# Performance work log

Measured on AMD Instinct MI355X. Metric: run time of the kernel, lower is better.

The kernel has to match this reference:

```python
import jax, jax.numpy as jnp
import numpy as np

B, S, H, I, E, K = 2, 2048, 1024, 2048, 8, 2


def setup_inputs() -> dict:
    key = jax.random.key(0)
    k1, k2, k3, k4, k5 = jax.random.split(key, 5)
    scale_h = 1.0 / np.sqrt(H)
    scale_i = 1.0 / np.sqrt(I)
    return {
        "x": jax.random.normal(k1, (B, S, H), dtype=jnp.float32),
        "Wg": jax.random.normal(k2, (H, E), dtype=jnp.float32) * scale_h,
        "W11": jax.random.normal(k3, (E, H, I), dtype=jnp.float32) * scale_h,
        "W12": jax.random.normal(k4, (E, H, I), dtype=jnp.float32) * scale_h,
        "W2": jax.random.normal(k5, (E, I, H), dtype=jnp.float32) * scale_i,
    }


def reference(x, Wg, W11, W12, W2):
    # Router: softmax over experts, then top-k with renormalization (+1e-8 as in torch ref)
    gate_scores = jax.nn.softmax(x @ Wg, axis=-1)          # [B,S,E]
    topk_scores, topk_idx = jax.lax.top_k(gate_scores, K)   # [B,S,K]
    topk_scores = topk_scores / (topk_scores.sum(-1, keepdims=True) + 1e-8)

    # Dense per-expert SwiGLU on all tokens (matches reference's masked-dense math)
    gate = jnp.einsum('bsh,ehi->bsei', x, W11)              # [B,S,E,I]
    value = jnp.einsum('bsh,ehi->bsei', x, W12)
    fused = (gate * jax.nn.sigmoid(gate)) * value           # SiLU(gate) * value
    expert_out = jnp.einsum('bsei,eih->bseh', fused, W2)    # [B,S,E,H]

    # Gather the top-k experts' outputs per token and combine with routing weights
    gathered = jnp.take_along_axis(expert_out, topk_idx[..., None], axis=2)  # [B,S,K,H]
    out = jnp.sum(topk_scores[..., None] * gathered, axis=2)                 # [B,S,H]
    return out
```

## Files before the change

### kernel.cpp

```cpp
#include <hip/hip_runtime.h>
#include <hip/hip_bf16.h>
#include <stdint.h>

#define B_ 2
#define S_ 2048
#define H_ 1024
#define I_ 2048
#define E_ 8
#define TOK (B_*S_)
#define PAIRS (TOK*2)
#define MAXBLK 80

typedef __bf16 bf16_t;
typedef __bf16 bf16x4 __attribute__((ext_vector_type(4)));
typedef __bf16 bf16x8 __attribute__((ext_vector_type(8)));
typedef float  f32x4  __attribute__((ext_vector_type(4)));
typedef float  f32x16 __attribute__((ext_vector_type(16)));

__device__ __forceinline__ void gl_lds16(const bf16_t* g, bf16_t* l) {
    __builtin_amdgcn_global_load_lds(
        (const __attribute__((address_space(1))) unsigned int*)g,
        (__attribute__((address_space(3))) unsigned int*)l, 16, 0, 0);
}

__global__ void router_kernel(const float* __restrict__ x, const float* __restrict__ Wg,
                              int* __restrict__ top2e, float* __restrict__ top2w,
                              int* __restrict__ counts) {
    int wave = threadIdx.x >> 6;
    int lane = threadIdx.x & 63;
    int t = blockIdx.x * 4 + wave;
    if (t >= TOK) return;
    float acc[E_];
#pragma unroll
    for (int e = 0; e < E_; e++) acc[e] = 0.f;
    const float* xrow = x + (size_t)t * H_;
    for (int j = 0; j < H_ / 64; j++) {
        int h = j * 64 + lane;
        float xv = xrow[h];
        const float4* wg = (const float4*)(Wg + (size_t)h * E_);
        float4 w0 = wg[0], w1 = wg[1];
        acc[0] += xv * w0.x; acc[1] += xv * w0.y; acc[2] += xv * w0.z; acc[3] += xv * w0.w;
        acc[4] += xv * w1.x; acc[5] += xv * w1.y; acc[6] += xv * w1.z; acc[7] += xv * w1.w;
    }
#pragma unroll
    for (int e = 0; e < E_; e++) {
#pragma unroll
        for (int m = 32; m >= 1; m >>= 1) acc[e] += __shfl_xor(acc[e], m, 64);
    }
    if (lane == 0) {
        float mx = acc[0];
        for (int e = 1; e < E_; e++) mx = fmaxf(mx, acc[e]);
        float p[E_]; float z = 0.f;
        for (int e = 0; e < E_; e++) { p[e] = __expf(acc[e] - mx); z += p[e]; }
        for (int e = 0; e < E_; e++) p[e] /= z;
        int i1 = 0; float p1 = p[0];
        for (int e = 1; e < E_; e++) if (p[e] > p1) { p1 = p[e]; i1 = e; }
        int i2 = -1; float p2 = -1.f;
        for (int e = 0; e < E_; e++) if (e != i1 && p[e] > p2) { p2 = p[e]; i2 = e; }
        float s = p1 + p2 + 1e-8f;
        top2e[t * 2]     = i1; top2e[t * 2 + 1] = i2;
        top2w[t * 2]     = p1 / s; top2w[t * 2 + 1] = p2 / s;
        atomicAdd(&counts[i1], 1);
        atomicAdd(&counts[i2], 1);
    }
}

__global__ void scan_kernel(const int* __restrict__ counts, int* __restrict__ offsets,
                            int* __restrict__ cursor, int* __restrict__ blk_e,
                            int* __restrict__ blk_m0, int* __restrict__ nblk) {
    if (threadIdx.x == 0 && blockIdx.x == 0) {
        int run = 0, b = 0;
        for (int e = 0; e < E_; e++) {
            offsets[e] = run; cursor[e] = run;
            int c = counts[e];
            for (int m0 = 0; m0 < c; m0 += 128) { blk_e[b] = e; blk_m0[b] = m0; b++; }
            run += c;
        }
        nblk[0] = b;
    }
}

__global__ void fill_kernel(const int* __restrict__ top2e,
                            int* __restrict__ cursor, int* __restrict__ pair_tok,
                            int* __restrict__ inv) {
    int t = blockIdx.x * blockDim.x + threadIdx.x;
    if (t >= TOK) return;
#pragma unroll
    for (int k = 0; k < 2; k++) {
        int e = top2e[t * 2 + k];
        int pos = atomicAdd(&cursor[e], 1);
        pair_tok[pos] = t;
        inv[t * 2 + k] = pos;
    }
}

__global__ void castx_kernel(const float* __restrict__ x, bf16_t* __restrict__ xb) {
    size_t i = ((size_t)blockIdx.x * blockDim.x + threadIdx.x) * 4;
    float4 v = *(const float4*)(x + i);
    bf16x4 o = { (bf16_t)v.x, (bf16_t)v.y, (bf16_t)v.z, (bf16_t)v.w };
    *(bf16x4*)(xb + i) = o;
}

__global__ __launch_bounds__(256) void transpose_cast_kernel(
    const float* __restrict__ src, bf16_t* __restrict__ dst, int R, int C) {
    __shared__ float tile[64][129];
    int e = blockIdx.z;
    const float* s = src + (size_t)e * R * C;
    bf16_t* d = dst + (size_t)e * R * C;
    int c0 = blockIdx.x * 128, r0 = blockIdx.y * 64;
    int t = threadIdx.x;
#pragma unroll
    for (int j = 0; j < 8; j++) {
        int flat = j * 256 + t;
        int r = flat >> 5;
        int c4 = (flat & 31) * 4;
        float4 v = *(const float4*)(s + (size_t)(r0 + r) * C + c0 + c4);
        tile[r][c4 + 0] = v.x;
        tile[r][c4 + 1] = v.y;
        tile[r][c4 + 2] = v.z;
        tile[r][c4 + 3] = v.w;
    }
    __syncthreads();
#pragma unroll
    for (int j = 0; j < 4; j++) {
        int flat = j * 256 + t;
        int orow = flat >> 3;
        int seg  = (flat & 7) * 8;
        bf16x8 v;
#pragma unroll
        for (int k = 0; k < 8; k++) v[k] = (bf16_t)tile[seg + k][orow];
        *(bf16x8*)(d + (size_t)(c0 + orow) * R + r0 + seg) = v;
    }
}

__global__ __launch_bounds__(256, 2) void gemm1_kernel(
    const bf16_t* __restrict__ xb,
    const bf16_t* __restrict__ W11t,
    const bf16_t* __restrict__ W12t,
    const int* __restrict__ counts, const int* __restrict__ offsets,
    const int* __restrict__ blk_e, const int* __restrict__ blk_m0,
    const int* __restrict__ nblk,
    const int* __restrict__ pair_tok,
    bf16_t* __restrict__ fused)
{
    int by = blockIdx.y;
    if (by >= nblk[0]) return;
    int e = blk_e[by];
    int m0 = blk_m0[by];
    int cnt = counts[e];
    int off = offsets[e];
    int n0 = blockIdx.x * 128;

    __shared__ __align__(16) bf16_t la[128 * 64];
    __shared__ __align__(16) bf16_t lb[256 * 64];

    int tid = threadIdx.x;
    int w = tid >> 6, lane = tid & 63;
    int wm = w >> 1, wn = w & 1;
    int lrow = lane >> 3, lcol = lane & 7;
    int scol = lcol ^ lrow;

    const bf16_t* aptr4[4];
    const bf16_t* bptr[8];
#pragma unroll
    for (int it = 0; it < 4; it++) {
        int r = it * 32 + w * 8 + lrow;
        int grow = m0 + r;
        int tok = pair_tok[off + (grow < cnt ? grow : 0)];
        aptr4[it] = xb + (size_t)tok * H_ + scol * 8;
    }
#pragma unroll
    for (int it = 0; it < 8; it++) {
        int r = it * 32 + w * 8 + lrow;
        const bf16_t* base = (r < 128)
            ? (W11t + ((size_t)e * I_ + n0 + r) * H_)
            : (W12t + ((size_t)e * I_ + n0 + (r - 128)) * H_);
        bptr[it] = base + scol * 8;
    }

    f32x16 acc[2][4];
#pragma unroll
    for (int a = 0; a < 2; a++)
#pragma unroll
        for (int b = 0; b < 4; b++) acc[a][b] = (f32x16)(0.f);

    int r32 = lane & 31;
    int khalf = lane >> 5;
    int rx = r32 & 7;

    for (int k0 = 0; k0 < H_; k0 += 64) {
#pragma unroll
        for (int it = 0; it < 4; it++)
            gl_lds16(aptr4[it] + k0, &la[(it * 32 + w * 8) * 64]);
#pragma unroll
        for (int it = 0; it < 8; it++)
            gl_lds16(bptr[it] + k0, &lb[(it * 32 + w * 8) * 64]);
        __syncthreads();
#pragma unroll
        for (int t16 = 0; t16 < 4; t16++) {
            int seg = t16 * 2 + khalf;
            bf16x8 af[2], bfr[4];
#pragma unroll
            for (int ms = 0; ms < 2; ms++) {
                int row = wm * 64 + ms * 32 + r32;
                af[ms] = *(const bf16x8*)&la[row * 64 + (seg ^ rx) * 8];
            }
#pragma unroll
            for (int ns = 0; ns < 2; ns++) {
                int browg = wn * 64 + ns * 32 + r32;
                bfr[ns]     = *(const bf16x8*)&lb[browg * 64 + (seg ^ rx) * 8];
                bfr[ns + 2] = *(const bf16x8*)&lb[(browg + 128) * 64 + (seg ^ rx) * 8];
            }
#pragma unroll
            for (int ms = 0; ms < 2; ms++)
#pragma unroll
                for (int ns = 0; ns < 4; ns++)
                    acc[ms][ns] = __builtin_amdgcn_mfma_f32_32x32x16_bf16(
                        af[ms], bfr[ns], acc[ms][ns], 0, 0, 0);
        }
        __syncthreads();
    }

#pragma unroll
    for (int ms = 0; ms < 2; ms++) {
#pragma unroll
        for (int ns = 0; ns < 2; ns++) {
            int i = n0 + wn * 64 + ns * 32 + r32;
#pragma unroll
            for (int reg = 0; reg < 16; reg++) {
                int rrow = (reg & 3) + 8 * (reg >> 2) + 4 * khalf;
                int grow = m0 + wm * 64 + ms * 32 + rrow;
                if (grow < cnt) {
                    float g = acc[ms][ns][reg];
                    float v = acc[ms][ns + 2][reg];
                    float f = g * v / (1.f + __expf(-g));
                    fused[(size_t)(off + grow) * I_ + i] = (bf16_t)f;
                }
            }
        }
    }
}

__global__ __launch_bounds__(256, 3) void gemm2_kernel(
    const bf16_t* __restrict__ fused,
    const bf16_t* __restrict__ W2t,
    const int* __restrict__ counts, const int* __restrict__ offsets,
    const int* __restrict__ blk_e, const int* __restrict__ blk_m0,
    const int* __restrict__ nblk,
    float* __restrict__ y)
{
    int by = blockIdx.y;
    if (by >= nblk[0]) return;
    int e = blk_e[by];
    int m0 = blk_m0[by];
    int cnt = counts[e];
    int off = offsets[e];
    int n0 = blockIdx.x * 128;

    __shared__ __align__(16) bf16_t la[128 * 64];
    __shared__ __align__(16) bf16_t lb[128 * 64];

    int tid = threadIdx.x;
    int w = tid >> 6, lane = tid & 63;
    int wm = w >> 1, wn = w & 1;
    int lrow = lane >> 3, lcol = lane & 7;
    int scol = lcol ^ lrow;

    const bf16_t* aptr[4];
    const bf16_t* bptr[4];
#pragma unroll
    for (int it = 0; it < 4; it++) {
        int r = it * 32 + w * 8 + lrow;
        int grow = m0 + r;
        if (grow >= cnt) grow = cnt - 1;
        aptr[it] = fused + (size_t)(off + grow) * I_ + scol * 8;
        bptr[it] = W2t + ((size_t)e * H_ + n0 + r) * I_ + scol * 8;
    }

    f32x16 acc[2][2];
#pragma unroll
    for (int a = 0; a < 2; a++)
#pragma unroll
        for (int b = 0; b < 2; b++) acc[a][b] = (f32x16)(0.f);

    int r32 = lane & 31;
    int khalf = lane >> 5;
    int rx = r32 & 7;

    for (int k0 = 0; k0 < I_; k0 += 64) {
#pragma unroll
        for (int it = 0; it < 4; it++) {
            gl_lds16(aptr[it] + k0, &la[(it * 32 + w * 8) * 64]);
            gl_lds16(bptr[it] + k0, &lb[(it * 32 + w * 8) * 64]);
        }
        __syncthreads();
#pragma unroll
        for (int t16 = 0; t16 < 4; t16++) {
            int seg = t16 * 2 + khalf;
            bf16x8 af[2], bfr[2];
#pragma unroll
            for (int ms = 0; ms < 2; ms++) {
                int row = wm * 64 + ms * 32 + r32;
                af[ms] = *(const bf16x8*)&la[row * 64 + (seg ^ rx) * 8];
            }
#pragma unroll
            for (int ns = 0; ns < 2; ns++) {
                int brow = wn * 64 + ns * 32 + r32;
                bfr[ns] = *(const bf16x8*)&lb[brow * 64 + (seg ^ rx) * 8];
            }
#pragma unroll
            for (int ms = 0; ms < 2; ms++)
#pragma unroll
                for (int ns = 0; ns < 2; ns++)
                    acc[ms][ns] = __builtin_amdgcn_mfma_f32_32x32x16_bf16(
                        af[ms], bfr[ns], acc[ms][ns], 0, 0, 0);
        }
        __syncthreads();
    }

#pragma unroll
    for (int ms = 0; ms < 2; ms++) {
#pragma unroll
        for (int reg = 0; reg < 16; reg++) {
            int rrow = (reg & 3) + 8 * (reg >> 2) + 4 * khalf;
            int grow = m0 + wm * 64 + ms * 32 + rrow;
            if (grow < cnt) {
                int slot = off + grow;
#pragma unroll
                for (int ns = 0; ns < 2; ns++) {
                    int h = n0 + wn * 64 + ns * 32 + r32;
                    y[(size_t)slot * H_ + h] = acc[ms][ns][reg];
                }
            }
        }
    }
}

__global__ __launch_bounds__(256) void combine_kernel(
    const float* __restrict__ y, const int* __restrict__ inv,
    const float* __restrict__ top2w, float* __restrict__ out) {
    int t = blockIdx.x;
    int h = threadIdx.x * 4;
    int s1 = inv[t * 2], s2 = inv[t * 2 + 1];
    float w1 = top2w[t * 2], w2 = top2w[t * 2 + 1];
    f32x4 a = *(const f32x4*)(y + (size_t)s1 * H_ + h);
    f32x4 b = *(const f32x4*)(y + (size_t)s2 * H_ + h);
    f32x4 r = a * w1 + b * w2;
    *(f32x4*)(out + (size_t)t * H_ + h) = r;
}

extern "C" void kernel_launch(void* const* d_in, const int* in_sizes, int n_in,
                              void* d_out, int out_size, void* d_ws, size_t ws_size,
                              hipStream_t stream) {
    const float* x   = (const float*)d_in[0];
    const float* Wg  = (const float*)d_in[1];
    const float* W11 = (const float*)d_in[2];
    const float* W12 = (const float*)d_in[3];
    const float* W2  = (const float*)d_in[4];
    float* out = (float*)d_out;

    char* ws = (char*)d_ws;
    size_t o = 0;
    auto alloc = [&](size_t bytes) { size_t r = o; o = (o + bytes + 255) & ~(size_t)255; return r; };
    int*    counts   = (int*)(ws + alloc(E_ * 4));
    int*    offsets  = (int*)(ws + alloc(E_ * 4));
    int*    cursor   = (int*)(ws + alloc(E_ * 4));
    int*    blk_e    = (int*)(ws + alloc(MAXBLK * 4));
    int*    blk_m0   = (int*)(ws + alloc(MAXBLK * 4));
    int*    nblk     = (int*)(ws + alloc(4));
    int*    top2e    = (int*)(ws + alloc(TOK * 2 * 4));
    float*  top2w    = (float*)(ws + alloc(TOK * 2 * 4));
    int*    pair_tok = (int*)(ws + alloc(PAIRS * 4));
    int*    inv      = (int*)(ws + alloc(TOK * 2 * 4));
    bf16_t* xb       = (bf16_t*)(ws + alloc((size_t)TOK * H_ * 2));
    bf16_t* W11t     = (bf16_t*)(ws + alloc((size_t)E_ * I_ * H_ * 2));
    bf16_t* W12t     = (bf16_t*)(ws + alloc((size_t)E_ * I_ * H_ * 2));
    bf16_t* W2t      = (bf16_t*)(ws + alloc((size_t)E_ * I_ * H_ * 2));
    bf16_t* fusedbuf = (bf16_t*)(ws + alloc((size_t)PAIRS * I_ * 2));
    float*  ybuf     = (float*)(ws + alloc((size_t)PAIRS * H_ * 4));

    hipMemsetAsync(counts, 0, E_ * 4, stream);

    router_kernel<<<TOK / 4, 256, 0, stream>>>(x, Wg, top2e, top2w, counts);
    scan_kernel<<<1, 64, 0, stream>>>(counts, offsets, cursor, blk_e, blk_m0, nblk);
    fill_kernel<<<TOK / 256, 256, 0, stream>>>(top2e, cursor, pair_tok, inv);

    castx_kernel<<<(TOK * H_ / 4) / 256, 256, 0, stream>>>(x, xb);
    transpose_cast_kernel<<<dim3(I_ / 128, H_ / 64, E_), 256, 0, stream>>>(W11, W11t, H_, I_);
    transpose_cast_kernel<<<dim3(I_ / 128, H_ / 64, E_), 256, 0, stream>>>(W12, W12t, H_, I_);
    transpose_cast_kernel<<<dim3(H_ / 128, I_ / 64, E_), 256, 0, stream>>>(W2, W2t, I_, H_);

    gemm1_kernel<<<dim3(I_ / 128, MAXBLK), 256, 0, stream>>>(
        xb, W11t, W12t, counts, offsets, blk_e, blk_m0, nblk, pair_tok, fusedbuf);
    gemm2_kernel<<<dim3(H_ / 128, MAXBLK), 256, 0, stream>>>(
        fusedbuf, W2t, counts, offsets, blk_e, blk_m0, nblk, ybuf);
    combine_kernel<<<TOK, 256, 0, stream>>>(ybuf, inv, top2w, out);
}
```

Measured before the change: 527.5 us.

## Fuse x cast into router, merge scan/fill and weight transposes, store y in bf16

```diff
diff --git a/kernel.cpp b/kernel.cpp
--- a/kernel.cpp
+++ b/kernel.cpp
@@ -25,7 +25,7 @@
 
 __global__ void router_kernel(const float* __restrict__ x, const float* __restrict__ Wg,
                               int* __restrict__ top2e, float* __restrict__ top2w,
-                              int* __restrict__ counts) {
+                              int* __restrict__ counts, bf16_t* __restrict__ xb) {
     int wave = threadIdx.x >> 6;
     int lane = threadIdx.x & 63;
     int t = blockIdx.x * 4 + wave;
@@ -41,6 +41,15 @@
         float4 w0 = wg[0], w1 = wg[1];
         acc[0] += xv * w0.x; acc[1] += xv * w0.y; acc[2] += xv * w0.z; acc[3] += xv * w0.w;
         acc[4] += xv * w1.x; acc[5] += xv * w1.y; acc[6] += xv * w1.z; acc[7] += xv * w1.w;
+    }
+#pragma unroll
+    for (int part = 0; part < 2; part++) {
+        int idx = part * 512 + lane * 8;
+        float4 v0 = *(const float4*)(xrow + idx);
+        float4 v1 = *(const float4*)(xrow + idx + 4);
+        bf16x8 ov = { (bf16_t)v0.x, (bf16_t)v0.y, (bf16_t)v0.z, (bf16_t)v0.w,
+                      (bf16_t)v1.x, (bf16_t)v1.y, (bf16_t)v1.z, (bf16_t)v1.w };
+        *(bf16x8*)(xb + (size_t)t * H_ + idx) = ov;
     }
 #pragma unroll
     for (int e = 0; e < E_; e++) {
@@ -65,49 +74,46 @@
     }
 }
 
-__global__ void scan_kernel(const int* __restrict__ counts, int* __restrict__ offsets,
-                            int* __restrict__ cursor, int* __restrict__ blk_e,
-                            int* __restrict__ blk_m0, int* __restrict__ nblk) {
-    if (threadIdx.x == 0 && blockIdx.x == 0) {
+__global__ __launch_bounds__(256) void scanfill_kernel(
+    const int* __restrict__ counts, int* __restrict__ offsets,
+    int* __restrict__ blk_e, int* __restrict__ blk_m0, int* __restrict__ nblk,
+    const int* __restrict__ top2e, int* __restrict__ pair_tok, int* __restrict__ inv) {
+    __shared__ int s_cur[E_];
+    if (threadIdx.x == 0) {
         int run = 0, b = 0;
         for (int e = 0; e < E_; e++) {
-            offsets[e] = run; cursor[e] = run;
+            offsets[e] = run; s_cur[e] = run;
             int c = counts[e];
             for (int m0 = 0; m0 < c; m0 += 128) { blk_e[b] = e; blk_m0[b] = m0; b++; }
             run += c;
         }
         nblk[0] = b;
     }
-}
-
-__global__ void fill_kernel(const int* __restrict__ top2e,
-                            int* __restrict__ cursor, int* __restrict__ pair_tok,
-                            int* __restrict__ inv) {
-    int t = blockIdx.x * blockDim.x + threadIdx.x;
-    if (t >= TOK) return;
-#pragma unroll
-    for (int k = 0; k < 2; k++) {
-        int e = top2e[t * 2 + k];
-        int pos = atomicAdd(&cursor[e], 1);
-        pair_tok[pos] = t;
-        inv[t * 2 + k] = pos;
-    }
-}
-
-__global__ void castx_kernel(const float* __restrict__ x, bf16_t* __restrict__ xb) {
-    size_t i = ((size_t)blockIdx.x * blockDim.x + threadIdx.x) * 4;
-    float4 v = *(const float4*)(x + i);
-    bf16x4 o = { (bf16_t)v.x, (bf16_t)v.y, (bf16_t)v.z, (bf16_t)v.w };
-    *(bf16x4*)(xb + i) = o;
-}
-
-__global__ __launch_bounds__(256) void transpose_cast_kernel(
-    const float* __restrict__ src, bf16_t* __restrict__ dst, int R, int C) {
+    __syncthreads();
+    for (int p = threadIdx.x; p < PAIRS; p += 256) {
+        int e = top2e[p];
+        int pos = atomicAdd(&s_cur[e], 1);
+        pair_tok[pos] = p >> 1;
+        inv[p] = pos;
+    }
+}
+
+__global__ __launch_bounds__(256) void wtrans_kernel(
+    const float* __restrict__ W11, const float* __restrict__ W12,
+    const float* __restrict__ W2,
+    bf16_t* __restrict__ W11t, bf16_t* __restrict__ W12t, bf16_t* __restrict__ W2t) {
     __shared__ float tile[64][129];
-    int e = blockIdx.z;
-    const float* s = src + (size_t)e * R * C;
-    bf16_t* d = dst + (size_t)e * R * C;
-    int c0 = blockIdx.x * 128, r0 = blockIdx.y * 64;
+    int z = blockIdx.y;
+    int wsel = z >> 3, e = z & 7;
+    const float* sbase; bf16_t* dbase; int R, C, tx, ty;
+    if (wsel == 0)      { sbase = W11; dbase = W11t; R = H_; C = I_; }
+    else if (wsel == 1) { sbase = W12; dbase = W12t; R = H_; C = I_; }
+    else                { sbase = W2;  dbase = W2t;  R = I_; C = H_; }
+    if (wsel < 2) { tx = blockIdx.x & 15; ty = blockIdx.x >> 4; }
+    else          { tx = blockIdx.x & 7;  ty = blockIdx.x >> 3; }
+    const float* s = sbase + (size_t)e * R * C;
+    bf16_t* d = dbase + (size_t)e * R * C;
+    int c0 = tx * 128, r0 = ty * 64;
     int t = threadIdx.x;
 #pragma unroll
     for (int j = 0; j < 8; j++) {
@@ -247,7 +253,7 @@
     const int* __restrict__ counts, const int* __restrict__ offsets,
     const int* __restrict__ blk_e, const int* __restrict__ blk_m0,
     const int* __restrict__ nblk,
-    float* __restrict__ y)
+    bf16_t* __restrict__ y)
 {
     int by = blockIdx.y;
     if (by >= nblk[0]) return;
@@ -329,7 +335,7 @@
 #pragma unroll
                 for (int ns = 0; ns < 2; ns++) {
                     int h = n0 + wn * 64 + ns * 32 + r32;
-                    y[(size_t)slot * H_ + h] = acc[ms][ns][reg];
+                    y[(size_t)slot * H_ + h] = (bf16_t)acc[ms][ns][reg];
                 }
             }
         }
@@ -337,15 +343,17 @@
 }
 
 __global__ __launch_bounds__(256) void combine_kernel(
-    const float* __restrict__ y, const int* __restrict__ inv,
+    const bf16_t* __restrict__ y, const int* __restrict__ inv,
     const float* __restrict__ top2w, float* __restrict__ out) {
     int t = blockIdx.x;
     int h = threadIdx.x * 4;
     int s1 = inv[t * 2], s2 = inv[t * 2 + 1];
     float w1 = top2w[t * 2], w2 = top2w[t * 2 + 1];
-    f32x4 a = *(const f32x4*)(y + (size_t)s1 * H_ + h);
-    f32x4 b = *(const f32x4*)(y + (size_t)s2 * H_ + h);
-    f32x4 r = a * w1 + b * w2;
+    bf16x4 a = *(const bf16x4*)(y + (size_t)s1 * H_ + h);
+    bf16x4 b = *(const bf16x4*)(y + (size_t)s2 * H_ + h);
+    f32x4 r;
+#pragma unroll
+    for (int k = 0; k < 4; k++) r[k] = w1 * (float)a[k] + w2 * (float)b[k];
     *(f32x4*)(out + (size_t)t * H_ + h) = r;
 }
 
@@ -364,7 +372,6 @@
     auto alloc = [&](size_t bytes) { size_t r = o; o = (o + bytes + 255) & ~(size_t)255; return r; };
     int*    counts   = (int*)(ws + alloc(E_ * 4));
     int*    offsets  = (int*)(ws + alloc(E_ * 4));
-    int*    cursor   = (int*)(ws + alloc(E_ * 4));
     int*    blk_e    = (int*)(ws + alloc(MAXBLK * 4));
     int*    blk_m0   = (int*)(ws + alloc(MAXBLK * 4));
     int*    nblk     = (int*)(ws + alloc(4));
@@ -377,18 +384,14 @@
     bf16_t* W12t     = (bf16_t*)(ws + alloc((size_t)E_ * I_ * H_ * 2));
     bf16_t* W2t      = (bf16_t*)(ws + alloc((size_t)E_ * I_ * H_ * 2));
     bf16_t* fusedbuf = (bf16_t*)(ws + alloc((size_t)PAIRS * I_ * 2));
-    float*  ybuf     = (float*)(ws + alloc((size_t)PAIRS * H_ * 4));
+    bf16_t* ybuf     = (bf16_t*)(ws + alloc((size_t)PAIRS * H_ * 2));
 
     hipMemsetAsync(counts, 0, E_ * 4, stream);
 
-    router_kernel<<<TOK / 4, 256, 0, stream>>>(x, Wg, top2e, top2w, counts);
-    scan_kernel<<<1, 64, 0, stream>>>(counts, offsets, cursor, blk_e, blk_m0, nblk);
-    fill_kernel<<<TOK / 256, 256, 0, stream>>>(top2e, cursor, pair_tok, inv);
-
-    castx_kernel<<<(TOK * H_ / 4) / 256, 256, 0, stream>>>(x, xb);
-    transpose_cast_kernel<<<dim3(I_ / 128, H_ / 64, E_), 256, 0, stream>>>(W11, W11t, H_, I_);
-    transpose_cast_kernel<<<dim3(I_ / 128, H_ / 64, E_), 256, 0, stream>>>(W12, W12t, H_, I_);
-    transpose_cast_kernel<<<dim3(H_ / 128, I_ / 64, E_), 256, 0, stream>>>(W2, W2t, I_, H_);
+    router_kernel<<<TOK / 4, 256, 0, stream>>>(x, Wg, top2e, top2w, counts, xb);
+    scanfill_kernel<<<1, 256, 0, stream>>>(counts, offsets, blk_e, blk_m0, nblk,
+                                           top2e, pair_tok, inv);
+    wtrans_kernel<<<dim3(256, 24), 256, 0, stream>>>(W11, W12, W2, W11t, W12t, W2t);
 
     gemm1_kernel<<<dim3(I_ / 128, MAXBLK), 256, 0, stream>>>(
         xb, W11t, W12t, counts, offsets, blk_e, blk_m0, nblk, pair_tok, fusedbuf);
```

After: 497.1 us. 5.8% less time.
